# Kernel optimization log

Hardware: AMD Instinct MI355X
Metric: run time of the kernel (lower is better)

Reference implementation:

```python
import jax, jax.numpy as jnp
import numpy as np

B, N, DIM, H, DH = 2, 1024, 1024, 8, 64
DI = H * DH  # 512
K = 4        # depthwise conv kernel
EPS = 1.1920929e-07  # float32 eps (torch RMSNorm default)


def setup_inputs() -> dict:
    key = jax.random.key(0)
    ks = jax.random.split(key, 12)
    s = lambda k, shape, sc=0.02: jax.random.normal(k, shape, jnp.float32) * sc
    return dict(
        x=jax.random.normal(ks[0], (B, N, DIM), jnp.float32),
        w_rms=jnp.ones((DIM,), jnp.float32),
        wq=s(ks[1], (DIM, DI)), wk=s(ks[2], (DIM, DI)), wv=s(ks[3], (DIM, DI)),
        wo=s(ks[4], (DI, DIM)),
        conv_q=s(ks[5], (DIM, K), 0.3), conv_k=s(ks[6], (DIM, K), 0.3), conv_v=s(ks[7], (DIM, K), 0.3),
        gamma_q=jnp.ones((H, 1, DH), jnp.float32), gamma_k=jnp.ones((H, 1, DH), jnp.float32),
        lr_w=s(ks[8], (DIM, H)), lr_b=jnp.full((H,), -4.0, jnp.float32),
        decay_w=s(ks[9], (DIM, H)), decay_b=jnp.full((H,), 4.0, jnp.float32),
        mom_w=s(ks[10], (DIM, H)), mom_b=jnp.full((H,), 2.0, jnp.float32),
    )


def rmsnorm(x, w):
    return x * jax.lax.rsqrt(jnp.mean(x * x, -1, keepdims=True) + EPS) * w


def mh_rmsnorm(x, gamma):  # x: (b, h, n, d)
    rms = jnp.sqrt(jnp.sum(x * x, -1, keepdims=True)) * (DH ** -0.5)
    return x / jnp.maximum(rms, 1e-8) * gamma


def dwconv(x, w):  # x: (b, n, dim), w: (dim, K) depthwise, padding K//2 -> length n+1
    y = jax.lax.conv_general_dilated(
        x.transpose(0, 2, 1), w[:, None, :], (1,), [(K // 2, K // 2)],
        feature_group_count=DIM, dimension_numbers=('NCW', 'OIW', 'NCW'))
    return y.transpose(0, 2, 1)


def gated_scan(a, x):  # h_t = a_t h_{t-1} + x_t, h_{-1}=0; a:(bh,t), x:(bh,t,d,d)
    def combine(c1, c2):
        a1, x1 = c1
        a2, x2 = c2
        return a1 * a2, a2 * x1 + x2
    _, h = jax.lax.associative_scan(combine, (a[..., None, None], x), axis=1)
    return h


def reference(x, w_rms, wq, wk, wv, wo, conv_q, conv_k, conv_v,
              gamma_q, gamma_k, lr_w, lr_b, decay_w, decay_b, mom_w, mom_b):
    b, n, _ = x.shape
    xa = rmsnorm(x, w_rms)
    qi, ki, vi = dwconv(xa, conv_q), dwconv(xa, conv_k), dwconv(xa, conv_v)
    split = lambda t: t.reshape(b, -1, H, DH).transpose(0, 2, 1, 3)[:, :, :n]  # (b,h,n,d)
    q = mh_rmsnorm(split(qi @ wq), gamma_q)
    k = mh_rmsnorm(split(ki @ wk), gamma_k)
    v = split(vi @ wv)
    fq = q.reshape(b * H, n, DH)
    fk = k.reshape(b * H, n, DH)
    fv = v.reshape(b * H, n, DH)
    sig = jax.nn.sigmoid
    lr = sig(xa @ lr_w + lr_b).transpose(0, 2, 1).reshape(b * H, n)
    decay = sig(xa @ decay_w + decay_b).transpose(0, 2, 1).reshape(b * H, n)
    mom = sig(xa @ mom_w + mom_b).transpose(0, 2, 1).reshape(b * H, n)
    # S_ref = S0 = 0 (fresh state) => pred = 0, delta_vec = -v
    g = jnp.einsum('bti,btj->btij', -fv, fk)          # (bh, n, d, d)
    Z = gated_scan(mom, g)                             # momentum scan
    S = gated_scan(decay, -lr[..., None, None] * Z)    # memory scan
    S_prev = jnp.concatenate([jnp.zeros_like(S[:, :1]), S[:, :-1]], axis=1)
    y = jnp.einsum('btdp,btp->btd', S_prev, fq)        # retrieval y_t = S_{t-1} psi_t
    y = y.reshape(b, H, n, DH).transpose(0, 2, 1, 3).reshape(b, n, DI)
    return y @ wo
```

## Files before the change

kernel.cpp:

```cpp
#include <hip/hip_runtime.h>
#include <math.h>

#define DEV __device__ __forceinline__

constexpr int Bb   = 2;
constexpr int Seq  = 1024;
constexpr int Dim  = 1024;
constexpr int Hh   = 8;
constexpr int Dh   = 64;
constexpr int Di   = 512;
constexpr int BN   = Bb * Seq;
constexpr int NSEQ = Bb * Hh;
constexpr int CHUNK = 32;
constexpr int CLEN  = Seq / CHUNK;
constexpr float EPSV = 1.1920929e-07f;
constexpr int NT2  = 8;
constexpr int KSPL = 8;

typedef _Float16 half8 __attribute__((ext_vector_type(8)));
typedef float    f32x4 __attribute__((ext_vector_type(4)));

DEV float bf2f(unsigned short u) {
  union { unsigned int i; float f; } x; x.i = ((unsigned int)u) << 16; return x.f;
}
DEV unsigned short f2bf(float f) {
  union { float f; unsigned int i; } x; x.f = f;
  unsigned int r = x.i + 0x7fffu + ((x.i >> 16) & 1u);
  return (unsigned short)(r >> 16);
}
DEV float ldin(const void* p, int f32, size_t i) {
  if (f32) return ((const float*)p)[i];
  return bf2f(((const unsigned short*)p)[i]);
}
DEV int sniff_vote(const void* p, int n, int tid) {
  int j = 2 * tid, valid = 0, bad = 0;
  if (j < n) {
    valid = 1;
    float v = bf2f(((const unsigned short*)p)[j]);
    float a = fabsf(v);
    if (!(a >= 1e-12f && a <= 1e4f)) bad = 1;
  }
#pragma unroll
  for (int m = 1; m < 64; m <<= 1) { valid += __shfl_xor(valid, m); bad += __shfl_xor(bad, m); }
  return (2 * bad > valid) ? 1 : 0;
}

struct InPtrs { const void* p[17]; int n[17]; };

__global__ __launch_bounds__(256) void k_prep_all(
    InPtrs ip,
    int* __restrict__ flags,
    _Float16* __restrict__ wqT, _Float16* __restrict__ wkT,
    _Float16* __restrict__ wvT, _Float16* __restrict__ woT,
    _Float16* __restrict__ WgT,
    _Float16* __restrict__ wcq, _Float16* __restrict__ wck,
    _Float16* __restrict__ wcv,
    float* __restrict__ gqf, float* __restrict__ gkf, float* __restrict__ gbf)
{
  int blk = blockIdx.x;
  int tid = threadIdx.x;
  __shared__ int sfl[8];

  if (blk < 1024) {
    int z = blk >> 8, bx = blk & 15, by = (blk >> 4) & 15;
    int idx = (z == 0) ? 2 : ((z == 1) ? 3 : ((z == 2) ? 4 : 5));
    const void* src = ip.p[idx];
    _Float16* dst   = (z == 0) ? wqT : ((z == 1) ? wkT : ((z == 2) ? wvT : woT));
    int Kd = (z < 3) ? Dim : Di;
    int Nn = (z < 3) ? Di : Dim;
    int n0 = bx * 64, k0 = by * 64;
    if (n0 >= Nn || k0 >= Kd) return;

    if (tid < 64) { int f = sniff_vote(src, ip.n[idx], tid); if (tid == 0) sfl[0] = f; }
    __syncthreads();
    int f = sfl[0];

    __shared__ float tile[64][65];
    int r = tid >> 4, c4 = (tid & 15) * 4;
#pragma unroll
    for (int rr = 0; rr < 4; ++rr) {
      int k = rr * 16 + r;
#pragma unroll
      for (int j = 0; j < 4; ++j)
        tile[k][c4 + j] = ldin(src, f, (size_t)(k0 + k) * Nn + n0 + c4 + j);
    }
    __syncthreads();
#pragma unroll
    for (int rr = 0; rr < 4; ++rr) {
      int n = rr * 16 + r;
      _Float16 o4[4];
#pragma unroll
      for (int j = 0; j < 4; ++j) o4[j] = (_Float16)tile[c4 + j][n];
      *(ushort4*)&dst[(size_t)(n0 + n) * Kd + k0 + c4] = *(ushort4*)o4;
    }
  } else if (blk < 1088) {
    int row = blk - 1024;
    if (row < 24) {
      int g = row >> 3, h = row & 7;
      int idx = (g == 0) ? 11 : ((g == 1) ? 13 : 15);
      const void* W = ip.p[idx];
      if (tid < 64) { int f = sniff_vote(W, ip.n[idx], tid); if (tid == 0) sfl[0] = f; }
      __syncthreads();
      int f = sfl[0];
#pragma unroll
      for (int it = 0; it < 4; ++it) {
        int d = it * 256 + tid;
        WgT[(size_t)row * Dim + d] = (_Float16)ldin(W, f, (size_t)d * Hh + h);
      }
    } else {
#pragma unroll
      for (int it = 0; it < 4; ++it)
        WgT[(size_t)row * Dim + it * 256 + tid] = (_Float16)0.f;
    }
  } else if (blk < 1104) {
    if (tid < 64) {
      int f6 = sniff_vote(ip.p[6], ip.n[6], tid);
      int f7 = sniff_vote(ip.p[7], ip.n[7], tid);
      int f8 = sniff_vote(ip.p[8], ip.n[8], tid);
      if (tid == 0) { sfl[0] = f6; sfl[1] = f7; sfl[2] = f8; }
    }
    __syncthreads();
    int e = (blk - 1088) * 256 + tid;
    wcq[e] = (_Float16)ldin(ip.p[6], sfl[0], e);
    wck[e] = (_Float16)ldin(ip.p[7], sfl[1], e);
    wcv[e] = (_Float16)ldin(ip.p[8], sfl[2], e);
  } else {
    __shared__ int allf[17];
    for (int ii = 0; ii < 17; ++ii) {
      if (tid < 64) {
        int f = sniff_vote(ip.p[ii], ip.n[ii], tid);
        if (tid == 0) { flags[ii] = f; allf[ii] = f; }
      }
    }
    __syncthreads();
    int f9 = allf[9], f10 = allf[10];
    for (int i = tid; i < Di; i += 256) {
      gqf[i] = ldin(ip.p[9], f9, i);
      gkf[i] = ldin(ip.p[10], f10, i);
    }
    if (tid < 24) {
      int g = tid >> 3, h = tid & 7;
      int idx = (g == 0) ? 12 : ((g == 1) ? 14 : 16);
      gbf[tid] = ldin(ip.p[idx], allf[idx], h);
    }
  }
}

__global__ __launch_bounds__(256) void k_rmsconv(
    const void* __restrict__ x, const void* __restrict__ w_rms,
    const int* __restrict__ flags,
    const _Float16* __restrict__ wcq, const _Float16* __restrict__ wck,
    const _Float16* __restrict__ wcv,
    _Float16* __restrict__ xaf,
    _Float16* __restrict__ qc, _Float16* __restrict__ kc,
    _Float16* __restrict__ vc)
{
  constexpr int NR = NT2 + 3;
  __shared__ _Float16 xas[NR][Dim];
  __shared__ float red[4];
  int tb = blockIdx.x, b = blockIdx.y;
  int t0 = tb * NT2;
  int tid = threadIdx.x, lane = tid & 63, wid = tid >> 6;
  int c0 = tid * 4;
  int fx = flags[0], fw = flags[1];

  float w0, w1, w2, w3;
  if (fw) {
    float4 u = *(const float4*)((const float*)w_rms + c0);
    w0 = u.x; w1 = u.y; w2 = u.z; w3 = u.w;
  } else {
    ushort4 u = *(const ushort4*)((const unsigned short*)w_rms + c0);
    w0 = bf2f(u.x); w1 = bf2f(u.y); w2 = bf2f(u.z); w3 = bf2f(u.w);
  }

  for (int rr = 0; rr < NR; ++rr) {
    int r = t0 - 2 + rr;
    float v0 = 0.f, v1 = 0.f, v2 = 0.f, v3 = 0.f;
    bool inr = (r >= 0 && r < Seq);
    if (inr) {
      size_t rb = (size_t)(b * Seq + r) * Dim + c0;
      if (fx) {
        float4 u = *(const float4*)((const float*)x + rb);
        v0 = u.x; v1 = u.y; v2 = u.z; v3 = u.w;
      } else {
        ushort4 u = *(const ushort4*)((const unsigned short*)x + rb);
        v0 = bf2f(u.x); v1 = bf2f(u.y); v2 = bf2f(u.z); v3 = bf2f(u.w);
      }
    }
    float ss = v0 * v0 + v1 * v1 + v2 * v2 + v3 * v3;
#pragma unroll
    for (int m = 1; m < 64; m <<= 1) ss += __shfl_xor(ss, m);
    if (lane == 0) red[wid] = ss;
    __syncthreads();
    float scale = rsqrtf((red[0] + red[1] + red[2] + red[3]) * (1.0f / Dim) + EPSV);

    _Float16 t4[4] = {(_Float16)(v0 * scale * w0), (_Float16)(v1 * scale * w1),
                      (_Float16)(v2 * scale * w2), (_Float16)(v3 * scale * w3)};
    *(ushort4*)&xas[rr][c0] = *(ushort4*)t4;
    if (inr && r >= t0 && r < t0 + NT2)
      *(ushort4*)&xaf[(size_t)(b * Seq + r) * Dim + c0] = *(ushort4*)t4;
    __syncthreads();
  }

  _Float16 lwq[16], lwk[16], lwv[16];
  *(uint4*)&lwq[0] = *(const uint4*)&wcq[c0 * 4];
  *(uint4*)&lwq[8] = *(const uint4*)&wcq[c0 * 4 + 8];
  *(uint4*)&lwk[0] = *(const uint4*)&wck[c0 * 4];
  *(uint4*)&lwk[8] = *(const uint4*)&wck[c0 * 4 + 8];
  *(uint4*)&lwv[0] = *(const uint4*)&wcv[c0 * 4];
  *(uint4*)&lwv[8] = *(const uint4*)&wcv[c0 * 4 + 8];

#pragma unroll
  for (int tt = 0; tt < NT2; ++tt) {
    float rv[4][4];
#pragma unroll
    for (int k = 0; k < 4; ++k) {
      _Float16 hx[4];
      *(ushort4*)hx = *(const ushort4*)&xas[tt + k][c0];
#pragma unroll
      for (int j = 0; j < 4; ++j) rv[k][j] = (float)hx[j];
    }
    _Float16 tq[4], tk[4], tv[4];
#pragma unroll
    for (int j = 0; j < 4; ++j) {
      float aq = rv[0][j] * (float)lwq[j * 4 + 0] + rv[1][j] * (float)lwq[j * 4 + 1]
               + rv[2][j] * (float)lwq[j * 4 + 2] + rv[3][j] * (float)lwq[j * 4 + 3];
      float ak = rv[0][j] * (float)lwk[j * 4 + 0] + rv[1][j] * (float)lwk[j * 4 + 1]
               + rv[2][j] * (float)lwk[j * 4 + 2] + rv[3][j] * (float)lwk[j * 4 + 3];
      float av = rv[0][j] * (float)lwv[j * 4 + 0] + rv[1][j] * (float)lwv[j * 4 + 1]
               + rv[2][j] * (float)lwv[j * 4 + 2] + rv[3][j] * (float)lwv[j * 4 + 3];
      tq[j] = (_Float16)aq; tk[j] = (_Float16)ak; tv[j] = (_Float16)av;
    }
    size_t o = ((size_t)(b * Seq + t0 + tt)) * Dim + c0;
    *(ushort4*)&qc[o] = *(ushort4*)tq;
    *(ushort4*)&kc[o] = *(ushort4*)tk;
    *(ushort4*)&vc[o] = *(ushort4*)tv;
  }
}

__global__ __launch_bounds__(256) void k_gates(
    const _Float16* __restrict__ xaf, const _Float16* __restrict__ WgT,
    float* __restrict__ gpart)
{
  __shared__ __align__(16) _Float16 As[64][40];
  __shared__ __align__(16) _Float16 Bs[64][40];

  int tid = threadIdx.x, lane = tid & 63, wvid = tid >> 6;
  int m0 = blockIdx.x * 64, ks = blockIdx.y;
  int srow = tid >> 2, scol = (tid & 3) * 8;
  int mrow = lane & 15, quad = lane >> 4;
  int kbase = ks * (Dim / KSPL);

  f32x4 acc[4];
#pragma unroll
  for (int mi = 0; mi < 4; ++mi) acc[mi] = (f32x4){0.f, 0.f, 0.f, 0.f};

  for (int kt = kbase; kt < kbase + Dim / KSPL; kt += 32) {
    __syncthreads();
    *(uint4*)&As[srow][scol] = *(const uint4*)&xaf[(size_t)(m0 + srow) * Dim + kt + scol];
    *(uint4*)&Bs[srow][scol] = *(const uint4*)&WgT[(size_t)srow * Dim + kt + scol];
    __syncthreads();
    half8 bfr = *(const half8*)&Bs[wvid * 16 + mrow][quad * 8];
#pragma unroll
    for (int mi = 0; mi < 4; ++mi) {
      half8 afr = *(const half8*)&As[mi * 16 + mrow][quad * 8];
      acc[mi] = __builtin_amdgcn_mfma_f32_16x16x32_f16(afr, bfr, acc[mi], 0, 0, 0);
    }
  }

  int col = wvid * 16 + mrow;
  if (col < 24) {
#pragma unroll
    for (int mi = 0; mi < 4; ++mi) {
#pragma unroll
      for (int r2 = 0; r2 < 4; ++r2) {
        int row = m0 + mi * 16 + quad * 4 + r2;
        gpart[((size_t)ks * BN + row) * 32 + col] = acc[mi][r2];
      }
    }
  }
}

__global__ __launch_bounds__(256) void k_gemm_128(
    const _Float16* __restrict__ A0, const _Float16* __restrict__ A1,
    const _Float16* __restrict__ A2,
    const _Float16* __restrict__ B0, const _Float16* __restrict__ B1,
    const _Float16* __restrict__ B2,
    void* __restrict__ C0, void* __restrict__ C1, void* __restrict__ C2,
    const int* __restrict__ flags,
    int Nn, int Kd, int is_final)
{
  int z = blockIdx.z;
  const _Float16* A  = (z == 0) ? A0 : ((z == 1) ? A1 : A2);
  const _Float16* Bt = (z == 0) ? B0 : ((z == 1) ? B1 : B2);
  void* C = (z == 0) ? C0 : ((z == 1) ? C1 : C2);

  __shared__ __align__(16) _Float16 As[128][40];
  __shared__ __align__(16) _Float16 Bs[64][40];

  int tid = threadIdx.x, lane = tid & 63, wv = tid >> 6;
  int n0 = blockIdx.x * 64, m0 = blockIdx.y * 128;
  int mrow = lane & 15, quad = lane >> 4;
  int wm = wv * 32;

  int ar0 = tid >> 2, ac0 = (tid & 3) * 8;
  int ar1 = (tid + 256) >> 2;

  f32x4 acc[2][4];
#pragma unroll
  for (int mi = 0; mi < 2; ++mi)
#pragma unroll
    for (int ni = 0; ni < 4; ++ni) acc[mi][ni] = (f32x4){0.f, 0.f, 0.f, 0.f};

  for (int kt = 0; kt < Kd; kt += 32) {
    __syncthreads();
    *(uint4*)&As[ar0][ac0] = *(const uint4*)&A[(size_t)(m0 + ar0) * Kd + kt + ac0];
    *(uint4*)&As[ar1][ac0] = *(const uint4*)&A[(size_t)(m0 + ar1) * Kd + kt + ac0];
    *(uint4*)&Bs[ar0][ac0] = *(const uint4*)&Bt[(size_t)(n0 + ar0) * Kd + kt + ac0];
    __syncthreads();

    half8 bfr[4];
#pragma unroll
    for (int ni = 0; ni < 4; ++ni)
      bfr[ni] = *(const half8*)&Bs[ni * 16 + mrow][quad * 8];
#pragma unroll
    for (int mi = 0; mi < 2; ++mi) {
      half8 afr = *(const half8*)&As[wm + mi * 16 + mrow][quad * 8];
#pragma unroll
      for (int ni = 0; ni < 4; ++ni)
        acc[mi][ni] = __builtin_amdgcn_mfma_f32_16x16x32_f16(afr, bfr[ni], acc[mi][ni], 0, 0, 0);
    }
  }

  int any_bf16 = 0;
  if (is_final) {
#pragma unroll
    for (int i2 = 0; i2 < 17; ++i2) any_bf16 |= (flags[i2] == 0);
  }

#pragma unroll
  for (int mi = 0; mi < 2; ++mi) {
#pragma unroll
    for (int ni = 0; ni < 4; ++ni) {
      int col = n0 + ni * 16 + mrow;
#pragma unroll
      for (int r2 = 0; r2 < 4; ++r2) {
        int row = m0 + wm + mi * 16 + quad * 4 + r2;
        float v = acc[mi][ni][r2];
        size_t idx = (size_t)row * Nn + col;
        if (!is_final)        ((_Float16*)C)[idx] = (_Float16)v;
        else if (any_bf16)    ((unsigned short*)C)[idx] = f2bf(v);
        else                  ((float*)C)[idx] = v;
      }
    }
  }
}

DEV void load_gates(const float* __restrict__ gpart, const float* __restrict__ gbf,
                    int b, int h, int c, int tid,
                    float* gl, float* gd, float* gm)
{
  if (tid < 96) {
    int which = tid >> 5, t2 = tid & 31;
    int col = which * 8 + h;
    int row = b * Seq + c * CLEN + t2;
    float acc = gbf[col];
#pragma unroll
    for (int ks = 0; ks < KSPL; ++ks)
      acc += gpart[((size_t)ks * BN + row) * 32 + col];
    float sg = 1.f / (1.f + expf(-acc));
    if (which == 0) gl[t2] = sg; else if (which == 1) gd[t2] = sg; else gm[t2] = sg;
  }
}

__global__ __launch_bounds__(256) void k_phaseA(
    const _Float16* __restrict__ kpre, const _Float16* __restrict__ vpre,
    const float* __restrict__ gkf,
    const float* __restrict__ gpart, const float* __restrict__ gbf,
    _Float16* __restrict__ ZS_Z, _Float16* __restrict__ ZS_S,
    float* __restrict__ Mc, float* __restrict__ Dc, float* __restrict__ Wc)
{
  int c = blockIdx.x, s = blockIdx.y;
  int b = s >> 3, h = s & 7;
  int tid = threadIdx.x, lane = tid & 63, wv = tid >> 6;
  int i = tid >> 2, j0 = (tid & 3) * 16;
  __shared__ float kn[CLEN][64], vv[CLEN][64];
  __shared__ float gl[CLEN], gd[CLEN], gm[CLEN];

  {
    int t = tid >> 3, col = (tid & 7) * 8;
    size_t g = ((size_t)(b * Seq + c * CLEN + t)) * Di + h * 64 + col;
    half8 kv = *(const half8*)&kpre[g];
    half8 vvv = *(const half8*)&vpre[g];
#pragma unroll
    for (int j = 0; j < 8; ++j) { kn[t][col + j] = (float)kv[j]; vv[t][col + j] = (float)vvv[j]; }
    load_gates(gpart, gbf, b, h, c, tid, gl, gd, gm);
  }
  __syncthreads();
  {
    float gk = gkf[h * 64 + lane];
#pragma unroll
    for (int tt = 0; tt < 8; ++tt) {
      int t = wv * 8 + tt;
      float kvv = kn[t][lane];
      float ss = kvv * kvv;
#pragma unroll
      for (int m = 1; m < 64; m <<= 1) ss += __shfl_xor(ss, m);
      kn[t][lane] = kvv * (1.f / fmaxf(sqrtf(ss) * 0.125f, 1e-8f)) * gk;
    }
  }
  __syncthreads();

  float Zl[16], Sl[16];
#pragma unroll
  for (int jj = 0; jj < 16; ++jj) { Zl[jj] = 0.f; Sl[jj] = 0.f; }
  float Mcum = 1.f, Dcum = 1.f, wacc = 0.f;

  for (int t = 0; t < CLEN; ++t) {
    float l = gl[t], dd = gd[t], mm = gm[t];
    float vi = vv[t][i];
    Mcum *= mm;
#pragma unroll
    for (int jj = 0; jj < 16; ++jj) {
      Zl[jj] = fmaf(mm, Zl[jj], -vi * kn[t][j0 + jj]);
      Sl[jj] = fmaf(dd, Sl[jj], -l * Zl[jj]);
    }
    wacc = fmaf(dd, wacc, -l * Mcum);
    Dcum *= dd;
  }
  size_t base = ((size_t)(s * CHUNK + c)) * 4096 + (size_t)i * 64 + j0;
  half8 zo0, zo1, so0, so1;
#pragma unroll
  for (int jj = 0; jj < 8; ++jj) {
    zo0[jj] = (_Float16)Zl[jj];     zo1[jj] = (_Float16)Zl[jj + 8];
    so0[jj] = (_Float16)Sl[jj];     so1[jj] = (_Float16)Sl[jj + 8];
  }
  *(half8*)&ZS_Z[base] = zo0; *(half8*)&ZS_Z[base + 8] = zo1;
  *(half8*)&ZS_S[base] = so0; *(half8*)&ZS_S[base + 8] = so1;
  if (tid == 0) {
    Mc[s * CHUNK + c] = Mcum; Dc[s * CHUNK + c] = Dcum; Wc[s * CHUNK + c] = wacc;
  }
}

__global__ __launch_bounds__(256) void k_phaseB(
    _Float16* __restrict__ ZS_Z, _Float16* __restrict__ ZS_S,
    const float* __restrict__ Mc, const float* __restrict__ Dc,
    const float* __restrict__ Wc)
{
  int s = blockIdx.x;
  int e = blockIdx.y * 256 + threadIdx.x;
  float Z = 0.f, S = 0.f;
  for (int c = 0; c < CHUNK; ++c) {
    size_t base = ((size_t)(s * CHUNK + c)) * 4096 + e;
    float mc = Mc[s * CHUNK + c], dc = Dc[s * CHUNK + c], wc = Wc[s * CHUNK + c];
    float zl = (float)ZS_Z[base], sl = (float)ZS_S[base];
    ZS_Z[base] = (_Float16)Z; ZS_S[base] = (_Float16)S;
    S = fmaf(dc, S, fmaf(wc, Z, sl));
    Z = fmaf(mc, Z, zl);
  }
}

__global__ __launch_bounds__(256) void k_phaseC(
    const _Float16* __restrict__ qpre, const _Float16* __restrict__ kpre,
    const _Float16* __restrict__ vpre,
    const float* __restrict__ gqf, const float* __restrict__ gkf,
    const float* __restrict__ gpart, const float* __restrict__ gbf,
    const _Float16* __restrict__ ZS_Z, const _Float16* __restrict__ ZS_S,
    _Float16* __restrict__ yb)
{
  int c = blockIdx.x, s = blockIdx.y;
  int b = s >> 3, h = s & 7;
  int tid = threadIdx.x, lane = tid & 63, wv = tid >> 6;
  int i = tid >> 2, j0 = (tid & 3) * 16;
  __shared__ float kn[CLEN][64], vv[CLEN][64], qn[CLEN][64];
  __shared__ float gl[CLEN], gd[CLEN], gm[CLEN];

  float Zi_[16], Si_[16], Zl[16], Sl[16];
  size_t base = ((size_t)(s * CHUNK + c)) * 4096 + (size_t)i * 64 + j0;
  {
    half8 z0 = *(const half8*)&ZS_Z[base], z1 = *(const half8*)&ZS_Z[base + 8];
    half8 s0 = *(const half8*)&ZS_S[base], s1 = *(const half8*)&ZS_S[base + 8];
#pragma unroll
    for (int jj = 0; jj < 8; ++jj) {
      Zi_[jj] = (float)z0[jj]; Zi_[jj + 8] = (float)z1[jj];
      Si_[jj] = (float)s0[jj]; Si_[jj + 8] = (float)s1[jj];
      Zl[jj] = 0.f; Zl[jj + 8] = 0.f; Sl[jj] = 0.f; Sl[jj + 8] = 0.f;
    }
  }
  {
    int t = tid >> 3, col = (tid & 7) * 8;
    size_t g = ((size_t)(b * Seq + c * CLEN + t)) * Di + h * 64 + col;
    half8 kv = *(const half8*)&kpre[g];
    half8 vvv = *(const half8*)&vpre[g];
    half8 qv = *(const half8*)&qpre[g];
#pragma unroll
    for (int j = 0; j < 8; ++j) {
      kn[t][col + j] = (float)kv[j]; vv[t][col + j] = (float)vvv[j];
      qn[t][col + j] = (float)qv[j];
    }
    load_gates(gpart, gbf, b, h, c, tid, gl, gd, gm);
  }
  __syncthreads();
  {
    float gk = gkf[h * 64 + lane];
    float gq = gqf[h * 64 + lane];
#pragma unroll
    for (int tt = 0; tt < 8; ++tt) {
      int t = wv * 8 + tt;
      float kvv = kn[t][lane];
      float ssk = kvv * kvv;
      float qvv = qn[t][lane];
      float ssq = qvv * qvv;
#pragma unroll
      for (int m = 1; m < 64; m <<= 1) { ssk += __shfl_xor(ssk, m); ssq += __shfl_xor(ssq, m); }
      kn[t][lane] = kvv * (1.f / fmaxf(sqrtf(ssk) * 0.125f, 1e-8f)) * gk;
      qn[t][lane] = qvv * (1.f / fmaxf(sqrtf(ssq) * 0.125f, 1e-8f)) * gq;
    }
  }
  __syncthreads();

  float Mcum = 1.f, Dcum = 1.f, wacc = 0.f;
  float Dprev = 1.f, wprev = 0.f;

  for (int t = 0; t < CLEN; ++t) {
    float l = gl[t], dd = gd[t], mm = gm[t];

    float yp = 0.f;
#pragma unroll
    for (int jj = 0; jj < 16; ++jj) {
      float tmp = fmaf(Dprev, Si_[jj], fmaf(wprev, Zi_[jj], Sl[jj]));
      yp = fmaf(tmp, qn[t][j0 + jj], yp);
    }
    yp += __shfl_xor(yp, 1);
    yp += __shfl_xor(yp, 2);
    if ((tid & 3) == 0)
      yb[((size_t)(b * Seq + c * CLEN + t)) * Di + h * 64 + i] = (_Float16)yp;

    float vi = vv[t][i];
    Mcum *= mm;
#pragma unroll
    for (int jj = 0; jj < 16; ++jj) {
      Zl[jj] = fmaf(mm, Zl[jj], -vi * kn[t][j0 + jj]);
      Sl[jj] = fmaf(dd, Sl[jj], -l * Zl[jj]);
    }
    wacc = fmaf(dd, wacc, -l * Mcum);
    Dcum *= dd;
    Dprev = Dcum; wprev = wacc;
  }
}

extern "C" void kernel_launch(void* const* d_in, const int* in_sizes, int n_in,
                              void* d_out, int out_size, void* d_ws, size_t ws_size,
                              hipStream_t stream) {
  InPtrs ip;
  for (int i = 0; i < 17; ++i) { ip.p[i] = d_in[i]; ip.n[i] = in_sizes[i]; }

  char* p = (char*)d_ws;
  auto take = [&](size_t bytes) -> char* {
    char* q = p; p += (bytes + 255) & ~(size_t)255; return q;
  };
  int* flags           = (int*)take(32 * 4);
  _Float16* xaf        = (_Float16*)take((size_t)BN * Dim * 2);
  _Float16* qc         = (_Float16*)take((size_t)BN * Dim * 2);
  _Float16* kc         = (_Float16*)take((size_t)BN * Dim * 2);
  _Float16* vc         = (_Float16*)take((size_t)BN * Dim * 2);
  _Float16* qpre       = (_Float16*)take((size_t)BN * Di * 2);
  _Float16* kpre       = (_Float16*)take((size_t)BN * Di * 2);
  _Float16* vpre       = (_Float16*)take((size_t)BN * Di * 2);
  float* gpart         = (float*)take((size_t)KSPL * BN * 32 * 4);
  float* Mc            = (float*)take((size_t)NSEQ * CHUNK * 4);
  float* Dc            = (float*)take((size_t)NSEQ * CHUNK * 4);
  float* Wc            = (float*)take((size_t)NSEQ * CHUNK * 4);
  _Float16* wqT        = (_Float16*)take((size_t)Di * Dim * 2);
  _Float16* wkT        = (_Float16*)take((size_t)Di * Dim * 2);
  _Float16* wvT        = (_Float16*)take((size_t)Di * Dim * 2);
  _Float16* woT        = (_Float16*)take((size_t)Dim * Di * 2);
  _Float16* WgT        = (_Float16*)take((size_t)64 * Dim * 2);
  _Float16* wcq        = (_Float16*)take((size_t)Dim * 4 * 2);
  _Float16* wck        = (_Float16*)take((size_t)Dim * 4 * 2);
  _Float16* wcv        = (_Float16*)take((size_t)Dim * 4 * 2);
  float* gqf           = (float*)take(Di * 4);
  float* gkf           = (float*)take(Di * 4);
  float* gbf           = (float*)take(32 * 4);
  _Float16* ZS_Z       = qc;
  _Float16* ZS_S       = kc;
  _Float16* yb         = vc;

  k_prep_all<<<1105, 256, 0, stream>>>(ip, flags, wqT, wkT, wvT, woT, WgT,
                                       wcq, wck, wcv, gqf, gkf, gbf);

  k_rmsconv<<<dim3(Seq / NT2, Bb), 256, 0, stream>>>(
      d_in[0], d_in[1], flags, wcq, wck, wcv, xaf, qc, kc, vc);

  k_gates<<<dim3(BN / 64, KSPL), 256, 0, stream>>>(xaf, WgT, gpart);

  dim3 g1(Di / 64, BN / 128, 3);
  k_gemm_128<<<g1, 256, 0, stream>>>(qc, kc, vc, wqT, wkT, wvT,
                                     qpre, kpre, vpre, flags, Di, Dim, 0);

  k_phaseA<<<dim3(CHUNK, NSEQ), 256, 0, stream>>>(kpre, vpre, gkf,
                                                  gpart, gbf,
                                                  ZS_Z, ZS_S, Mc, Dc, Wc);
  k_phaseB<<<dim3(NSEQ, 16), 256, 0, stream>>>(ZS_Z, ZS_S, Mc, Dc, Wc);
  k_phaseC<<<dim3(CHUNK, NSEQ), 256, 0, stream>>>(qpre, kpre, vpre, gqf, gkf,
                                                  gpart, gbf,
                                                  ZS_Z, ZS_S, yb);

  dim3 g2(Dim / 64, BN / 128, 1);
  k_gemm_128<<<g2, 256, 0, stream>>>(yb, yb, yb, woT, woT, woT,
                                     d_out, d_out, d_out, flags, Dim, Di, 1);
}
```

Measured before the change: 195.6 us.

## Merge gate and QKV GEMMs into one launch; per-wave RMSNorm rows

The gate projection GEMM and the three Q/K/V projection GEMMs now run in a single kernel. Blocks 0-383 compute the Q/K/V tiles and blocks 384-639 compute the split-K gate partials, which removes one launch and lets the two independent workloads share the GPU. In the RMSNorm+conv kernel, each wave now normalizes a whole row with 16 elements per lane and a wave-level reduction. This drops the two block-wide barriers per row. The prep transpose uses vectorized 4-element loads, and the final GEMM is specialized so it no longer branches on an is_final flag.

```diff
diff --git a/kernel.cpp b/kernel.cpp
--- a/kernel.cpp
+++ b/kernel.cpp
@@ -32,6 +32,15 @@
   if (f32) return ((const float*)p)[i];
   return bf2f(((const unsigned short*)p)[i]);
 }
+DEV void ld4(const void* p, int f32, size_t i, float* dst) {
+  if (f32) {
+    float4 u = *(const float4*)((const float*)p + i);
+    dst[0] = u.x; dst[1] = u.y; dst[2] = u.z; dst[3] = u.w;
+  } else {
+    ushort4 u = *(const ushort4*)((const unsigned short*)p + i);
+    dst[0] = bf2f(u.x); dst[1] = bf2f(u.y); dst[2] = bf2f(u.z); dst[3] = bf2f(u.w);
+  }
+}
 DEV int sniff_vote(const void* p, int n, int tid) {
   int j = 2 * tid, valid = 0, bad = 0;
   if (j < n) {
@@ -80,9 +89,7 @@
 #pragma unroll
     for (int rr = 0; rr < 4; ++rr) {
       int k = rr * 16 + r;
-#pragma unroll
-      for (int j = 0; j < 4; ++j)
-        tile[k][c4 + j] = ldin(src, f, (size_t)(k0 + k) * Nn + n0 + c4 + j);
+      ld4(src, f, (size_t)(k0 + k) * Nn + n0 + c4, &tile[k][c4]);
     }
     __syncthreads();
 #pragma unroll
@@ -157,51 +164,49 @@
 {
   constexpr int NR = NT2 + 3;
   __shared__ _Float16 xas[NR][Dim];
-  __shared__ float red[4];
   int tb = blockIdx.x, b = blockIdx.y;
   int t0 = tb * NT2;
-  int tid = threadIdx.x, lane = tid & 63, wid = tid >> 6;
-  int c0 = tid * 4;
+  int tid = threadIdx.x, lane = tid & 63, wv = tid >> 6;
   int fx = flags[0], fw = flags[1];
-
-  float w0, w1, w2, w3;
-  if (fw) {
-    float4 u = *(const float4*)((const float*)w_rms + c0);
-    w0 = u.x; w1 = u.y; w2 = u.z; w3 = u.w;
-  } else {
-    ushort4 u = *(const ushort4*)((const unsigned short*)w_rms + c0);
-    w0 = bf2f(u.x); w1 = bf2f(u.y); w2 = bf2f(u.z); w3 = bf2f(u.w);
-  }
-
-  for (int rr = 0; rr < NR; ++rr) {
+  int e0 = lane * 16;
+
+  float wr[16];
+#pragma unroll
+  for (int q = 0; q < 4; ++q) ld4(w_rms, fw, e0 + q * 4, &wr[q * 4]);
+
+  for (int rr = wv; rr < NR; rr += 4) {
     int r = t0 - 2 + rr;
-    float v0 = 0.f, v1 = 0.f, v2 = 0.f, v3 = 0.f;
+    float xv[16];
     bool inr = (r >= 0 && r < Seq);
     if (inr) {
-      size_t rb = (size_t)(b * Seq + r) * Dim + c0;
-      if (fx) {
-        float4 u = *(const float4*)((const float*)x + rb);
-        v0 = u.x; v1 = u.y; v2 = u.z; v3 = u.w;
-      } else {
-        ushort4 u = *(const ushort4*)((const unsigned short*)x + rb);
-        v0 = bf2f(u.x); v1 = bf2f(u.y); v2 = bf2f(u.z); v3 = bf2f(u.w);
-      }
-    }
-    float ss = v0 * v0 + v1 * v1 + v2 * v2 + v3 * v3;
+      size_t rb = (size_t)(b * Seq + r) * Dim + e0;
+#pragma unroll
+      for (int q = 0; q < 4; ++q) ld4(x, fx, rb + q * 4, &xv[q * 4]);
+    } else {
+#pragma unroll
+      for (int j = 0; j < 16; ++j) xv[j] = 0.f;
+    }
+    float ss = 0.f;
+#pragma unroll
+    for (int j = 0; j < 16; ++j) ss = fmaf(xv[j], xv[j], ss);
 #pragma unroll
     for (int m = 1; m < 64; m <<= 1) ss += __shfl_xor(ss, m);
-    if (lane == 0) red[wid] = ss;
-    __syncthreads();
-    float scale = rsqrtf((red[0] + red[1] + red[2] + red[3]) * (1.0f / Dim) + EPSV);
-
-    _Float16 t4[4] = {(_Float16)(v0 * scale * w0), (_Float16)(v1 * scale * w1),
-                      (_Float16)(v2 * scale * w2), (_Float16)(v3 * scale * w3)};
-    *(ushort4*)&xas[rr][c0] = *(ushort4*)t4;
-    if (inr && r >= t0 && r < t0 + NT2)
-      *(ushort4*)&xaf[(size_t)(b * Seq + r) * Dim + c0] = *(ushort4*)t4;
-    __syncthreads();
-  }
-
+    float scale = rsqrtf(ss * (1.0f / Dim) + EPSV);
+
+    _Float16 o[16];
+#pragma unroll
+    for (int j = 0; j < 16; ++j) o[j] = (_Float16)(xv[j] * scale * wr[j]);
+    *(uint4*)&xas[rr][e0]     = *(uint4*)&o[0];
+    *(uint4*)&xas[rr][e0 + 8] = *(uint4*)&o[8];
+    if (inr && r >= t0 && r < t0 + NT2) {
+      size_t ob = (size_t)(b * Seq + r) * Dim + e0;
+      *(uint4*)&xaf[ob]     = *(uint4*)&o[0];
+      *(uint4*)&xaf[ob + 8] = *(uint4*)&o[8];
+    }
+  }
+  __syncthreads();
+
+  int c0 = tid * 4;
   _Float16 lwq[16], lwk[16], lwv[16];
   *(uint4*)&lwq[0] = *(const uint4*)&wcq[c0 * 4];
   *(uint4*)&lwq[8] = *(const uint4*)&wcq[c0 * 4 + 8];
@@ -238,63 +243,113 @@
   }
 }
 
-__global__ __launch_bounds__(256) void k_gates(
+__global__ __launch_bounds__(256) void k_mid(
+    const _Float16* __restrict__ qc, const _Float16* __restrict__ kc,
+    const _Float16* __restrict__ vc,
+    const _Float16* __restrict__ wqT, const _Float16* __restrict__ wkT,
+    const _Float16* __restrict__ wvT,
     const _Float16* __restrict__ xaf, const _Float16* __restrict__ WgT,
+    _Float16* __restrict__ qpre, _Float16* __restrict__ kpre,
+    _Float16* __restrict__ vpre,
     float* __restrict__ gpart)
 {
-  __shared__ __align__(16) _Float16 As[64][40];
+  __shared__ __align__(16) _Float16 As[128][40];
   __shared__ __align__(16) _Float16 Bs[64][40];
 
-  int tid = threadIdx.x, lane = tid & 63, wvid = tid >> 6;
-  int m0 = blockIdx.x * 64, ks = blockIdx.y;
-  int srow = tid >> 2, scol = (tid & 3) * 8;
+  int blk = blockIdx.x;
+  int tid = threadIdx.x, lane = tid & 63, wv = tid >> 6;
   int mrow = lane & 15, quad = lane >> 4;
-  int kbase = ks * (Dim / KSPL);
-
-  f32x4 acc[4];
-#pragma unroll
-  for (int mi = 0; mi < 4; ++mi) acc[mi] = (f32x4){0.f, 0.f, 0.f, 0.f};
-
-  for (int kt = kbase; kt < kbase + Dim / KSPL; kt += 32) {
-    __syncthreads();
-    *(uint4*)&As[srow][scol] = *(const uint4*)&xaf[(size_t)(m0 + srow) * Dim + kt + scol];
-    *(uint4*)&Bs[srow][scol] = *(const uint4*)&WgT[(size_t)srow * Dim + kt + scol];
-    __syncthreads();
-    half8 bfr = *(const half8*)&Bs[wvid * 16 + mrow][quad * 8];
-#pragma unroll
-    for (int mi = 0; mi < 4; ++mi) {
-      half8 afr = *(const half8*)&As[mi * 16 + mrow][quad * 8];
-      acc[mi] = __builtin_amdgcn_mfma_f32_16x16x32_f16(afr, bfr, acc[mi], 0, 0, 0);
-    }
-  }
-
-  int col = wvid * 16 + mrow;
-  if (col < 24) {
-#pragma unroll
-    for (int mi = 0; mi < 4; ++mi) {
-#pragma unroll
-      for (int r2 = 0; r2 < 4; ++r2) {
-        int row = m0 + mi * 16 + quad * 4 + r2;
-        gpart[((size_t)ks * BN + row) * 32 + col] = acc[mi][r2];
+
+  if (blk < 384) {
+    int z = blk / 128, rem = blk - z * 128;
+    int by = rem >> 3, bx = rem & 7;
+    const _Float16* A  = (z == 0) ? qc : ((z == 1) ? kc : vc);
+    const _Float16* Bt = (z == 0) ? wqT : ((z == 1) ? wkT : wvT);
+    _Float16* C        = (z == 0) ? qpre : ((z == 1) ? kpre : vpre);
+    int n0 = bx * 64, m0 = by * 128;
+    int wm = wv * 32;
+    int ar0 = tid >> 2, ac0 = (tid & 3) * 8;
+    int ar1 = (tid + 256) >> 2;
+
+    f32x4 acc[2][4];
+#pragma unroll
+    for (int mi = 0; mi < 2; ++mi)
+#pragma unroll
+      for (int ni = 0; ni < 4; ++ni) acc[mi][ni] = (f32x4){0.f, 0.f, 0.f, 0.f};
+
+    for (int kt = 0; kt < Dim; kt += 32) {
+      __syncthreads();
+      *(uint4*)&As[ar0][ac0] = *(const uint4*)&A[(size_t)(m0 + ar0) * Dim + kt + ac0];
+      *(uint4*)&As[ar1][ac0] = *(const uint4*)&A[(size_t)(m0 + ar1) * Dim + kt + ac0];
+      *(uint4*)&Bs[ar0][ac0] = *(const uint4*)&Bt[(size_t)(n0 + ar0) * Dim + kt + ac0];
+      __syncthreads();
+
+      half8 bfr[4];
+#pragma unroll
+      for (int ni = 0; ni < 4; ++ni)
+        bfr[ni] = *(const half8*)&Bs[ni * 16 + mrow][quad * 8];
+#pragma unroll
+      for (int mi = 0; mi < 2; ++mi) {
+        half8 afr = *(const half8*)&As[wm + mi * 16 + mrow][quad * 8];
+#pragma unroll
+        for (int ni = 0; ni < 4; ++ni)
+          acc[mi][ni] = __builtin_amdgcn_mfma_f32_16x16x32_f16(afr, bfr[ni], acc[mi][ni], 0, 0, 0);
       }
     }
-  }
-}
-
-__global__ __launch_bounds__(256) void k_gemm_128(
-    const _Float16* __restrict__ A0, const _Float16* __restrict__ A1,
-    const _Float16* __restrict__ A2,
-    const _Float16* __restrict__ B0, const _Float16* __restrict__ B1,
-    const _Float16* __restrict__ B2,
-    void* __restrict__ C0, void* __restrict__ C1, void* __restrict__ C2,
-    const int* __restrict__ flags,
-    int Nn, int Kd, int is_final)
-{
-  int z = blockIdx.z;
-  const _Float16* A  = (z == 0) ? A0 : ((z == 1) ? A1 : A2);
-  const _Float16* Bt = (z == 0) ? B0 : ((z == 1) ? B1 : B2);
-  void* C = (z == 0) ? C0 : ((z == 1) ? C1 : C2);
-
+
+#pragma unroll
+    for (int mi = 0; mi < 2; ++mi) {
+#pragma unroll
+      for (int ni = 0; ni < 4; ++ni) {
+        int col = n0 + ni * 16 + mrow;
+#pragma unroll
+        for (int r2 = 0; r2 < 4; ++r2) {
+          int row = m0 + wm + mi * 16 + quad * 4 + r2;
+          C[(size_t)row * Di + col] = (_Float16)acc[mi][ni][r2];
+        }
+      }
+    }
+  } else {
+    int g = blk - 384;
+    int m0 = (g & 31) * 64, ks = g >> 5;
+    int srow = tid >> 2, scol = (tid & 3) * 8;
+    int kbase = ks * (Dim / KSPL);
+
+    f32x4 acc[4];
+#pragma unroll
+    for (int mi = 0; mi < 4; ++mi) acc[mi] = (f32x4){0.f, 0.f, 0.f, 0.f};
+
+    for (int kt = kbase; kt < kbase + Dim / KSPL; kt += 32) {
+      __syncthreads();
+      *(uint4*)&As[srow][scol] = *(const uint4*)&xaf[(size_t)(m0 + srow) * Dim + kt + scol];
+      *(uint4*)&Bs[srow][scol] = *(const uint4*)&WgT[(size_t)srow * Dim + kt + scol];
+      __syncthreads();
+      half8 bfr = *(const half8*)&Bs[wv * 16 + mrow][quad * 8];
+#pragma unroll
+      for (int mi = 0; mi < 4; ++mi) {
+        half8 afr = *(const half8*)&As[mi * 16 + mrow][quad * 8];
+        acc[mi] = __builtin_amdgcn_mfma_f32_16x16x32_f16(afr, bfr, acc[mi], 0, 0, 0);
+      }
+    }
+
+    int col = wv * 16 + mrow;
+    if (col < 24) {
+#pragma unroll
+      for (int mi = 0; mi < 4; ++mi) {
+#pragma unroll
+        for (int r2 = 0; r2 < 4; ++r2) {
+          int row = m0 + mi * 16 + quad * 4 + r2;
+          gpart[((size_t)ks * BN + row) * 32 + col] = acc[mi][r2];
+        }
+      }
+    }
+  }
+}
+
+__global__ __launch_bounds__(256) void k_gemm_fin(
+    const _Float16* __restrict__ A, const _Float16* __restrict__ Bt,
+    void* __restrict__ C, const int* __restrict__ flags, int Nn, int Kd)
+{
   __shared__ __align__(16) _Float16 As[128][40];
   __shared__ __align__(16) _Float16 Bs[64][40];
 
@@ -302,7 +357,6 @@
   int n0 = blockIdx.x * 64, m0 = blockIdx.y * 128;
   int mrow = lane & 15, quad = lane >> 4;
   int wm = wv * 32;
-
   int ar0 = tid >> 2, ac0 = (tid & 3) * 8;
   int ar1 = (tid + 256) >> 2;
 
@@ -333,10 +387,8 @@
   }
 
   int any_bf16 = 0;
-  if (is_final) {
-#pragma unroll
-    for (int i2 = 0; i2 < 17; ++i2) any_bf16 |= (flags[i2] == 0);
-  }
+#pragma unroll
+  for (int i2 = 0; i2 < 17; ++i2) any_bf16 |= (flags[i2] == 0);
 
 #pragma unroll
   for (int mi = 0; mi < 2; ++mi) {
@@ -348,9 +400,8 @@
         int row = m0 + wm + mi * 16 + quad * 4 + r2;
         float v = acc[mi][ni][r2];
         size_t idx = (size_t)row * Nn + col;
-        if (!is_final)        ((_Float16*)C)[idx] = (_Float16)v;
-        else if (any_bf16)    ((unsigned short*)C)[idx] = f2bf(v);
-        else                  ((float*)C)[idx] = v;
+        if (any_bf16) ((unsigned short*)C)[idx] = f2bf(v);
+        else          ((float*)C)[idx] = v;
       }
     }
   }
@@ -592,11 +643,8 @@
   k_rmsconv<<<dim3(Seq / NT2, Bb), 256, 0, stream>>>(
       d_in[0], d_in[1], flags, wcq, wck, wcv, xaf, qc, kc, vc);
 
-  k_gates<<<dim3(BN / 64, KSPL), 256, 0, stream>>>(xaf, WgT, gpart);
-
-  dim3 g1(Di / 64, BN / 128, 3);
-  k_gemm_128<<<g1, 256, 0, stream>>>(qc, kc, vc, wqT, wkT, wvT,
-                                     qpre, kpre, vpre, flags, Di, Dim, 0);
+  k_mid<<<640, 256, 0, stream>>>(qc, kc, vc, wqT, wkT, wvT, xaf, WgT,
+                                 qpre, kpre, vpre, gpart);
 
   k_phaseA<<<dim3(CHUNK, NSEQ), 256, 0, stream>>>(kpre, vpre, gkf,
                                                   gpart, gbf,
@@ -606,7 +654,6 @@
                                                   gpart, gbf,
                                                   ZS_Z, ZS_S, yb);
 
-  dim3 g2(Dim / 64, BN / 128, 1);
-  k_gemm_128<<<g2, 256, 0, stream>>>(yb, yb, yb, woT, woT, woT,
-                                     d_out, d_out, d_out, flags, Dim, Di, 1);
-}
+  k_gemm_fin<<<dim3(Dim / 64, BN / 128), 256, 0, stream>>>(
+      yb, woT, d_out, flags, Dim, Di);
+}
```

Result: faster. 186.3 us (-4.8%).
